# Kernel tuning notes

Hardware: AMD Instinct MI355X
Metric: run time of the kernel (lower is better)

Reference implementation:

```python
import jax, jax.numpy as jnp
import numpy as np
from jax import lax

IN_CH, OUT_CH, K, STYLE_DIM = 512, 512, 3, 512
B, H, W = 16, 64, 64
SCALE = 1.0 / np.sqrt(IN_CH * K * K).astype(np.float32)
EPS = 1e-8


def setup_inputs() -> dict:
    key = jax.random.key(0)
    k1, k2, k3, k4 = jax.random.split(key, 4)
    return {
        "x": jax.random.normal(k1, (B, IN_CH, H, W), dtype=jnp.float32),
        "style": jax.random.normal(k2, (B, STYLE_DIM), dtype=jnp.float32),
        "weight": jax.random.normal(k3, (1, OUT_CH, IN_CH, K, K), dtype=jnp.float32),
        "mod_w": jax.random.normal(k4, (IN_CH, STYLE_DIM), dtype=jnp.float32) / np.sqrt(STYLE_DIM),
        "mod_b": jnp.ones((IN_CH,), dtype=jnp.float32),
    }


def reference(x, style, weight, mod_w, mod_b):
    b, cin, h, w = x.shape
    out_ch = weight.shape[1]
    k = weight.shape[-1]
    pad = k // 2
    # style projection: (B, in_channel)
    s = style @ mod_w.T + mod_b
    # modulated weight: (B, out, in, k, k)
    wmod = SCALE * weight * s[:, None, :, None, None]
    # demodulation: rsqrt of sum of squares over (in, kh, kw)
    demod = lax.rsqrt(jnp.sum(wmod * wmod, axis=(2, 3, 4)) + EPS)
    wmod = wmod * demod[:, :, None, None, None]
    # grouped conv with groups = batch
    wflat = wmod.reshape(b * out_ch, cin, k, k)
    xin = x.reshape(1, b * cin, h, w)
    out = lax.conv_general_dilated(
        xin, wflat,
        window_strides=(1, 1),
        padding=[(pad, pad), (pad, pad)],
        dimension_numbers=("NCHW", "OIHW", "NCHW"),
        feature_group_count=b,
    )
    return out.reshape(b, out_ch, h, w)
```

## Files before the change

kernel.cpp:

```cpp
#include <hip/hip_runtime.h>
#include <hip/hip_bf16.h>
#include <cstdint>
#include <cstddef>

typedef __bf16 bf16x8 __attribute__((ext_vector_type(8)));
typedef float f32x4 __attribute__((ext_vector_type(4)));
typedef float f32x16 __attribute__((ext_vector_type(16)));

#define MOD_SCALE 1.4731391e-02f
#define EPSF 1e-8f

__global__ __launch_bounds__(64) void k_style(
    const float* __restrict__ style, const float* __restrict__ mod_w,
    const float* __restrict__ mod_b, float* __restrict__ s)
{
  __shared__ float st[512];
  const int b = blockIdx.x >> 3, ig = blockIdx.x & 7;
  const int t = threadIdx.x;
  for (int k = t; k < 512; k += 64) st[k] = style[b*512 + k];
  __syncthreads();
  const int i = ig*64 + t;
  const float4* mw = (const float4*)(mod_w + (size_t)i*512);
  float acc = 0.f;
  #pragma unroll 8
  for (int j = 0; j < 128; ++j) {
    float4 v = mw[j];
    acc += v.x*st[4*j] + v.y*st[4*j+1] + v.z*st[4*j+2] + v.w*st[4*j+3];
  }
  s[b*512 + i] = acc + mod_b[i];
}

__global__ __launch_bounds__(256) void k_weight(
    const float* __restrict__ weight, float* __restrict__ w2,
    __hip_bfloat16* __restrict__ Wb)
{
  const int o = blockIdx.x, t = threadIdx.x;
  #pragma unroll
  for (int h = 0; h < 2; ++h) {
    const int i = t + h*256;
    const float* wp = weight + ((size_t)o*512 + i)*9;
    float sq = 0.f;
    #pragma unroll
    for (int kk = 0; kk < 9; ++kk) {
      float v = wp[kk];
      sq += v*v;
      Wb[((size_t)kk*512 + o)*512 + i] = __float2bfloat16(v * MOD_SCALE);
    }
    w2[(size_t)o*512 + i] = sq;
  }
}

__global__ __launch_bounds__(64) void k_demod(
    const float* __restrict__ s, const float* __restrict__ w2,
    float* __restrict__ demod)
{
  __shared__ float s2[512];
  const int b = blockIdx.x >> 3, og = blockIdx.x & 7;
  const int t = threadIdx.x;
  for (int k = t; k < 512; k += 64) { float a = s[b*512 + k]; s2[k] = a*a; }
  __syncthreads();
  const int o = og*64 + t;
  const float4* wp = (const float4*)(w2 + (size_t)o*512);
  float acc = 0.f;
  #pragma unroll 8
  for (int j = 0; j < 128; ++j) {
    float4 v = wp[j];
    acc += v.x*s2[4*j] + v.y*s2[4*j+1] + v.z*s2[4*j+2] + v.w*s2[4*j+3];
  }
  demod[b*512 + o] = rsqrtf(MOD_SCALE*MOD_SCALE*acc + EPSF);
}

__global__ __launch_bounds__(256) void k_xm(
    const float* __restrict__ x, const float* __restrict__ s,
    __hip_bfloat16* __restrict__ Xm)
{
  __shared__ __hip_bfloat16 T[64][72];
  const int bid = blockIdx.x;
  const int cb = bid & 7, y = (bid >> 3) & 63, b = bid >> 9;
  const int ic0 = cb*64;
  const int t = threadIdx.x;
  const int i = t >> 2;
  const int q = t & 3;
  const int x0 = q*16;
  const float sv = s[b*512 + ic0 + i];
  const float4* xp = (const float4*)(x + (size_t)(b*512 + ic0 + i)*4096 + y*64 + x0);
  float4 v[4] = {xp[0], xp[1], xp[2], xp[3]};
  __hip_bfloat16 tmp[16];
  #pragma unroll
  for (int j = 0; j < 4; ++j) {
    tmp[4*j+0] = __float2bfloat16(((const float*)&v[j])[0]*sv);
    tmp[4*j+1] = __float2bfloat16(((const float*)&v[j])[1]*sv);
    tmp[4*j+2] = __float2bfloat16(((const float*)&v[j])[2]*sv);
    tmp[4*j+3] = __float2bfloat16(((const float*)&v[j])[3]*sv);
  }
  *(float4*)&T[i][x0]     = *(const float4*)&tmp[0];
  *(float4*)&T[i][x0 + 8] = *(const float4*)&tmp[8];

  const float4 z4 = make_float4(0.f, 0.f, 0.f, 0.f);
  if (t < 16) {
    const int side = t >> 3, j = t & 7;
    float4* hz = (float4*)(Xm + (((size_t)(b*66 + (y+1))*66 + side*65)*512 + ic0 + j*8));
    *hz = z4;
  }
  if (y == 0) {
    for (int idx = t; idx < 528; idx += 256) {
      const int px = idx >> 3, j = idx & 7;
      float4* hz = (float4*)(Xm + (((size_t)(b*66 + 0)*66 + px)*512 + ic0 + j*8));
      *hz = z4;
    }
  }
  if (y == 63) {
    for (int idx = t; idx < 528; idx += 256) {
      const int px = idx >> 3, j = idx & 7;
      float4* hz = (float4*)(Xm + (((size_t)(b*66 + 65)*66 + px)*512 + ic0 + j*8));
      *hz = z4;
    }
  }

  __syncthreads();
  const int p = t >> 2;
  __hip_bfloat16 o16[16];
  #pragma unroll
  for (int cc = 0; cc < 16; ++cc) o16[cc] = T[q*16 + cc][p];
  __hip_bfloat16* dst = Xm + (((size_t)(b*66 + (y+1))*66 + (p+1))*512 + ic0 + q*16);
  *(float4*)dst       = *(const float4*)&o16[0];
  *(float4*)(dst + 8) = *(const float4*)&o16[8];
}

#define VMC(n) asm volatile("s_waitcnt vmcnt(" #n ")" ::: "memory")

__global__ __launch_bounds__(512, 2) void k_conv(
    const __hip_bfloat16* __restrict__ Wb,
    const __hip_bfloat16* __restrict__ Xm,
    const float* __restrict__ demod,
    float* __restrict__ out)
{
  __shared__ __hip_bfloat16 lds[2][2][16384];

  const int orig = blockIdx.x;
  const int swz = (orig & 7)*64 + (orig >> 3);
  const int b  = swz >> 5;
  const int nt = (swz & 31) >> 1;
  const int mt = swz & 1;
  const int o0 = mt*256, y0 = nt*4;

  const int tid = threadIdx.x;
  const int l = tid & 63;
  const int w = tid >> 6;
  const int wm = w >> 2;
  const int wn = w & 3;

  const int srow = tid >> 3;
  const int tq   = (tid & 7) ^ (srow & 7);
  const char* WbC = (const char*)Wb;
  const char* XmC = (const char*)Xm;

  int aoff[2], boff[2], ldst[2];
  #pragma unroll
  for (int it = 0; it < 2; ++it) {
    const int R  = it*64 + srow;
    const int gr = (R & 0x6F) | ((tq & 1) << 4);
    const int gc = ((tq & 6) | ((R >> 4) & 1)) << 4;
    aoff[it] = (o0 + gr)*1024 + gc;
    boff[it] = (((b*66 + y0 + 1 + (gr >> 6))*66) + (gr & 63) + 1)*1024 + gc;
    ldst[it] = it*8192 + w*1024;
  }

  const int rowb = ((l >> 5) << 4) | (l & 15);
  const int lb4  = (l >> 4) & 1;
  const int sB   = (l & 7) << 4;

  #define STAGE_A(tau, h, bfi) do { \
    const int u_ = ((tau) >> 3)*524288 + (h)*131072 + (((tau) & 7) << 7); \
    _Pragma("unroll") \
    for (int it_ = 0; it_ < 2; ++it_) \
      __builtin_amdgcn_global_load_lds( \
        (__attribute__((address_space(1))) void*)(WbC + u_ + aoff[it_]), \
        (__attribute__((address_space(3))) void*)((char*)&lds[bfi][0][0] + (h)*16384 + ldst[it_]), \
        16, 0, 0); \
  } while(0)

  #define STAGE_B(tau, h, bfi) do { \
    const int kk_ = (tau) >> 3; \
    const int dy_ = kk_/3 - 1, dx_ = kk_ - (kk_/3)*3 - 1; \
    const int u_ = (((h)*2 + dy_)*66 + dx_)*1024 + (((tau) & 7) << 7); \
    _Pragma("unroll") \
    for (int it_ = 0; it_ < 2; ++it_) \
      __builtin_amdgcn_global_load_lds( \
        (__attribute__((address_space(1))) void*)(XmC + u_ + boff[it_]), \
        (__attribute__((address_space(3))) void*)((char*)&lds[bfi][1][0] + (h)*16384 + ldst[it_]), \
        16, 0, 0); \
  } while(0)

  #define RD_A(Ab, MH, dst) do { \
    _Pragma("unroll") \
    for (int mi_ = 0; mi_ < 2; ++mi_) \
      _Pragma("unroll") \
      for (int ks_ = 0; ks_ < 4; ++ks_) \
        dst[mi_][ks_] = *(const bf16x8*)((Ab) + (MH)*16384 + wm*8192 + mi_*4096 \
            + rowb*128 + (((((ks_<<1)|lb4)) << 4) ^ sB)); \
  } while(0)

  #define RD_B(Bb, NH, dst) do { \
    _Pragma("unroll") \
    for (int ks_ = 0; ks_ < 4; ++ks_) \
      dst[ks_] = *(const bf16x8*)((Bb) + (NH)*16384 + wn*4096 \
          + rowb*128 + (((((ks_<<1)|lb4)) << 4) ^ sB)); \
  } while(0)

  #define MFMAQ(AM0, dstA, NH, dstB) do { \
    _Pragma("unroll") \
    for (int ks_ = 0; ks_ < 4; ++ks_) \
      _Pragma("unroll") \
      for (int mi_ = 0; mi_ < 2; ++mi_) \
        acc[(AM0)+mi_][NH] = __builtin_amdgcn_mfma_f32_32x32x16_bf16( \
            dstA[mi_][ks_], dstB[ks_], acc[(AM0)+mi_][NH], 0, 0, 0); \
  } while(0)

  #define TILE(BFI, S1, S2, S3, S4, VM1, VM4) do { \
    const char* Ab_ = (const char*)&lds[BFI][0][0]; \
    const char* Bb_ = (const char*)&lds[BFI][1][0]; \
    bf16x8 a0_[2][4], a1_[2][4], b0_[4], b1_[4]; \
     \
    RD_A(Ab_, 0, a0_); RD_B(Bb_, 0, b0_); \
    S1; \
    __builtin_amdgcn_s_barrier(); \
    __builtin_amdgcn_s_setprio(1); MFMAQ(0, a0_, 0, b0_); __builtin_amdgcn_s_setprio(0); \
    VM1; \
    __builtin_amdgcn_s_barrier(); \
     \
    RD_B(Bb_, 1, b1_); \
    S2; \
    __builtin_amdgcn_s_barrier(); \
    __builtin_amdgcn_s_setprio(1); MFMAQ(0, a0_, 1, b1_); __builtin_amdgcn_s_setprio(0); \
    __builtin_amdgcn_s_barrier(); \
     \
    RD_A(Ab_, 1, a1_); \
    S3; \
    __builtin_amdgcn_s_barrier(); \
    __builtin_amdgcn_s_setprio(1); MFMAQ(2, a1_, 1, b1_); __builtin_amdgcn_s_setprio(0); \
    __builtin_amdgcn_s_barrier(); \
     \
    S4; \
    __builtin_amdgcn_s_barrier(); \
    __builtin_amdgcn_s_setprio(1); MFMAQ(2, a1_, 0, b0_); __builtin_amdgcn_s_setprio(0); \
    VM4; \
    __builtin_amdgcn_s_barrier(); \
  } while(0)

  f32x16 acc[4][2] = {};

  STAGE_A(0, 0, 0); STAGE_A(0, 1, 0); STAGE_B(0, 0, 0); STAGE_B(0, 1, 0);
  STAGE_B(1, 0, 1); STAGE_A(1, 1, 1);
  VMC(4);
  __builtin_amdgcn_s_barrier();

  #pragma unroll 1
  for (int tt = 0; tt < 35; ++tt) {
    const int t = tt*2;
    TILE(0, STAGE_A(t+1,0,1), STAGE_B(t+1,1,1), STAGE_B(t+2,0,0), STAGE_A(t+2,1,0),
            VMC(6), VMC(6));
    TILE(1, STAGE_A(t+2,0,0), STAGE_B(t+2,1,0), STAGE_B(t+3,0,1), STAGE_A(t+3,1,1),
            VMC(6), VMC(6));
  }
  TILE(0, STAGE_A(71,0,1), STAGE_B(71,1,1), (void)0, (void)0, VMC(6), VMC(2));
  TILE(1, (void)0, (void)0, (void)0, (void)0, VMC(0), (void)0);

  const int lr = l & 31;
  #pragma unroll
  for (int am = 0; am < 4; ++am) {
    const int om = o0 + (am >> 1)*128 + wm*64 + (am & 1)*32 + ((l >> 5) << 2);
    #pragma unroll
    for (int NH = 0; NH < 2; ++NH) {
      const int nc = NH*128 + wn*32 + lr;
      const int y = y0 + (nc >> 6), xx = nc & 63;
      #pragma unroll
      for (int g = 0; g < 4; ++g) {
        const f32x4 dm = *(const f32x4*)(demod + b*512 + om + 8*g);
        float* op = out + (size_t)(b*512 + om + 8*g)*4096 + y*64 + xx;
        #pragma unroll
        for (int j = 0; j < 4; ++j)
          op[(size_t)j*4096] = acc[am][NH][g*4 + j] * dm[j];
      }
    }
  }
  #undef TILE
  #undef MFMAQ
  #undef RD_A
  #undef RD_B
  #undef STAGE_A
  #undef STAGE_B
}

extern "C" void kernel_launch(void* const* d_in, const int* in_sizes, int n_in,
                              void* d_out, int out_size, void* d_ws, size_t ws_size,
                              hipStream_t stream)
{
  const float* x      = (const float*)d_in[0];
  const float* style  = (const float*)d_in[1];
  const float* weight = (const float*)d_in[2];
  const float* mod_w  = (const float*)d_in[3];
  const float* mod_b  = (const float*)d_in[4];
  float* out = (float*)d_out;

  char* ws = (char*)d_ws;
  float* s            = (float*)(ws);
  float* demod        = (float*)(ws + 32768);
  float* w2           = (float*)(ws + 65536);
  __hip_bfloat16* Wb  = (__hip_bfloat16*)(ws + 1114112);
  __hip_bfloat16* Xm  = (__hip_bfloat16*)(ws + 5832704);

  k_style <<<128,  64, 0, stream>>>(style, mod_w, mod_b, s);
  k_weight<<<512, 256, 0, stream>>>(weight, w2, Wb);
  k_demod <<<128,  64, 0, stream>>>(s, w2, demod);
  k_xm    <<<8192, 256, 0, stream>>>(x, s, Xm);
  k_conv  <<<512,  512, 0, stream>>>(Wb, Xm, demod, out);
}
```

Before: 352.6 us.

## Replace 256x256 conv GEMM tile with simpler 128x256 tile using 16x16 MFMA

Rewrites the main conv kernel to use 256-thread blocks computing 128 output channels by 256 pixels, with 16x16x32 MFMAs, a K-step of 32, and a simple double-buffered loop that waits for all loads and barriers every step. The grid is doubled to 1024 blocks. The old 512-thread, 256x256 tile with swizzled LDS, interleaved partial stages and priority hints is removed. This reduces register pressure and code complexity, but it also loses data reuse per block, adds bank conflicts from the unswizzled LDS layout, and puts a full vmcnt(0) wait plus a barrier in every one of the 144 iterations, so load latency is less hidden.

Result: slower. 369.8 us (+4.9%).

```diff
diff --git a/kernel.cpp b/kernel.cpp
--- a/kernel.cpp
+++ b/kernel.cpp
@@ -5,7 +5,6 @@
 
 typedef __bf16 bf16x8 __attribute__((ext_vector_type(8)));
 typedef float f32x4 __attribute__((ext_vector_type(4)));
-typedef float f32x16 __attribute__((ext_vector_type(16)));
 
 #define MOD_SCALE 1.4731391e-02f
 #define EPSF 1e-8f
@@ -129,167 +128,108 @@
 
 #define VMC(n) asm volatile("s_waitcnt vmcnt(" #n ")" ::: "memory")
 
-__global__ __launch_bounds__(512, 2) void k_conv(
+__global__ __launch_bounds__(256, 2) void k_conv(
     const __hip_bfloat16* __restrict__ Wb,
     const __hip_bfloat16* __restrict__ Xm,
     const float* __restrict__ demod,
     float* __restrict__ out)
 {
-  __shared__ __hip_bfloat16 lds[2][2][16384];
+  __shared__ __hip_bfloat16 lds[2][12288];
 
   const int orig = blockIdx.x;
-  const int swz = (orig & 7)*64 + (orig >> 3);
-  const int b  = swz >> 5;
-  const int nt = (swz & 31) >> 1;
-  const int mt = swz & 1;
-  const int o0 = mt*256, y0 = nt*4;
-
-  const int tid = threadIdx.x;
-  const int l = tid & 63;
-  const int w = tid >> 6;
-  const int wm = w >> 2;
-  const int wn = w & 3;
-
-  const int srow = tid >> 3;
-  const int tq   = (tid & 7) ^ (srow & 7);
+  const int swz = (orig & 7)*128 + (orig >> 3);
+  const int b  = swz >> 6;
+  const int mt = (swz >> 4) & 3;
+  const int nt = swz & 15;
+  const int o0 = mt*128, y0 = nt*4;
+
+  const int t = threadIdx.x;
+  const int l = t & 63;
+  const int w = t >> 6;
+
   const char* WbC = (const char*)Wb;
   const char* XmC = (const char*)Xm;
 
-  int aoff[2], boff[2], ldst[2];
-  #pragma unroll
-  for (int it = 0; it < 2; ++it) {
-    const int R  = it*64 + srow;
-    const int gr = (R & 0x6F) | ((tq & 1) << 4);
-    const int gc = ((tq & 6) | ((R >> 4) & 1)) << 4;
-    aoff[it] = (o0 + gr)*1024 + gc;
-    boff[it] = (((b*66 + y0 + 1 + (gr >> 6))*66) + (gr & 63) + 1)*1024 + gc;
-    ldst[it] = it*8192 + w*1024;
-  }
-
-  const int rowb = ((l >> 5) << 4) | (l & 15);
-  const int lb4  = (l >> 4) & 1;
-  const int sB   = (l & 7) << 4;
-
-  #define STAGE_A(tau, h, bfi) do { \
-    const int u_ = ((tau) >> 3)*524288 + (h)*131072 + (((tau) & 7) << 7); \
+  int aoff[2], boff[4];
+  #pragma unroll
+  for (int it = 0; it < 2; ++it)
+    aoff[it] = (o0 + it*64 + (t >> 2))*1024 + (t & 3)*16;
+  #pragma unroll
+  for (int it = 0; it < 4; ++it)
+    boff[it] = ((b*66 + y0 + 1 + it)*66 + (t >> 2) + 1)*1024 + (t & 3)*16;
+
+  const int fr  = l & 15;
+  const int kq  = (l >> 4) << 4;
+
+  #define STAGE(tau, bfi) do { \
+    const int ua_ = ((tau) >> 4)*524288 + (((tau) & 15) << 6); \
+    const int kk_ = (tau) >> 4; \
+    const int dy_ = kk_/3 - 1, dx_ = kk_ - (kk_/3)*3 - 1; \
+    const int ub_ = (dy_*66 + dx_)*1024 + (((tau) & 15) << 6); \
     _Pragma("unroll") \
     for (int it_ = 0; it_ < 2; ++it_) \
       __builtin_amdgcn_global_load_lds( \
-        (__attribute__((address_space(1))) void*)(WbC + u_ + aoff[it_]), \
-        (__attribute__((address_space(3))) void*)((char*)&lds[bfi][0][0] + (h)*16384 + ldst[it_]), \
+        (__attribute__((address_space(1))) void*)(WbC + ua_ + aoff[it_]), \
+        (__attribute__((address_space(3))) void*)((char*)&lds[bfi][0] + it_*4096 + w*1024), \
+        16, 0, 0); \
+    _Pragma("unroll") \
+    for (int it_ = 0; it_ < 4; ++it_) \
+      __builtin_amdgcn_global_load_lds( \
+        (__attribute__((address_space(1))) void*)(XmC + ub_ + boff[it_]), \
+        (__attribute__((address_space(3))) void*)((char*)&lds[bfi][0] + 8192 + it_*4096 + w*1024), \
         16, 0, 0); \
   } while(0)
 
-  #define STAGE_B(tau, h, bfi) do { \
-    const int kk_ = (tau) >> 3; \
-    const int dy_ = kk_/3 - 1, dx_ = kk_ - (kk_/3)*3 - 1; \
-    const int u_ = (((h)*2 + dy_)*66 + dx_)*1024 + (((tau) & 7) << 7); \
-    _Pragma("unroll") \
-    for (int it_ = 0; it_ < 2; ++it_) \
-      __builtin_amdgcn_global_load_lds( \
-        (__attribute__((address_space(1))) void*)(XmC + u_ + boff[it_]), \
-        (__attribute__((address_space(3))) void*)((char*)&lds[bfi][1][0] + (h)*16384 + ldst[it_]), \
-        16, 0, 0); \
+  #define COMPUTE(bfi) do { \
+    const char* Ab_ = (const char*)&lds[bfi][0]; \
+    const char* Bb_ = Ab_ + 8192; \
+    bf16x8 a_[8], b_[4]; \
+    _Pragma("unroll") \
+    for (int mi_ = 0; mi_ < 8; ++mi_) \
+      a_[mi_] = *(const bf16x8*)(Ab_ + (mi_*16 + fr)*64 + kq); \
+    _Pragma("unroll") \
+    for (int ni_ = 0; ni_ < 4; ++ni_) \
+      b_[ni_] = *(const bf16x8*)(Bb_ + (w*64 + ni_*16 + fr)*64 + kq); \
+    _Pragma("unroll") \
+    for (int mi_ = 0; mi_ < 8; ++mi_) \
+      _Pragma("unroll") \
+      for (int ni_ = 0; ni_ < 4; ++ni_) \
+        acc[mi_][ni_] = __builtin_amdgcn_mfma_f32_16x16x32_bf16( \
+            a_[mi_], b_[ni_], acc[mi_][ni_], 0, 0, 0); \
   } while(0)
 
-  #define RD_A(Ab, MH, dst) do { \
-    _Pragma("unroll") \
-    for (int mi_ = 0; mi_ < 2; ++mi_) \
-      _Pragma("unroll") \
-      for (int ks_ = 0; ks_ < 4; ++ks_) \
-        dst[mi_][ks_] = *(const bf16x8*)((Ab) + (MH)*16384 + wm*8192 + mi_*4096 \
-            + rowb*128 + (((((ks_<<1)|lb4)) << 4) ^ sB)); \
-  } while(0)
-
-  #define RD_B(Bb, NH, dst) do { \
-    _Pragma("unroll") \
-    for (int ks_ = 0; ks_ < 4; ++ks_) \
-      dst[ks_] = *(const bf16x8*)((Bb) + (NH)*16384 + wn*4096 \
-          + rowb*128 + (((((ks_<<1)|lb4)) << 4) ^ sB)); \
-  } while(0)
-
-  #define MFMAQ(AM0, dstA, NH, dstB) do { \
-    _Pragma("unroll") \
-    for (int ks_ = 0; ks_ < 4; ++ks_) \
-      _Pragma("unroll") \
-      for (int mi_ = 0; mi_ < 2; ++mi_) \
-        acc[(AM0)+mi_][NH] = __builtin_amdgcn_mfma_f32_32x32x16_bf16( \
-            dstA[mi_][ks_], dstB[ks_], acc[(AM0)+mi_][NH], 0, 0, 0); \
-  } while(0)
-
-  #define TILE(BFI, S1, S2, S3, S4, VM1, VM4) do { \
-    const char* Ab_ = (const char*)&lds[BFI][0][0]; \
-    const char* Bb_ = (const char*)&lds[BFI][1][0]; \
-    bf16x8 a0_[2][4], a1_[2][4], b0_[4], b1_[4]; \
-     \
-    RD_A(Ab_, 0, a0_); RD_B(Bb_, 0, b0_); \
-    S1; \
-    __builtin_amdgcn_s_barrier(); \
-    __builtin_amdgcn_s_setprio(1); MFMAQ(0, a0_, 0, b0_); __builtin_amdgcn_s_setprio(0); \
-    VM1; \
-    __builtin_amdgcn_s_barrier(); \
-     \
-    RD_B(Bb_, 1, b1_); \
-    S2; \
-    __builtin_amdgcn_s_barrier(); \
-    __builtin_amdgcn_s_setprio(1); MFMAQ(0, a0_, 1, b1_); __builtin_amdgcn_s_setprio(0); \
-    __builtin_amdgcn_s_barrier(); \
-     \
-    RD_A(Ab_, 1, a1_); \
-    S3; \
-    __builtin_amdgcn_s_barrier(); \
-    __builtin_amdgcn_s_setprio(1); MFMAQ(2, a1_, 1, b1_); __builtin_amdgcn_s_setprio(0); \
-    __builtin_amdgcn_s_barrier(); \
-     \
-    S4; \
-    __builtin_amdgcn_s_barrier(); \
-    __builtin_amdgcn_s_setprio(1); MFMAQ(2, a1_, 0, b0_); __builtin_amdgcn_s_setprio(0); \
-    VM4; \
-    __builtin_amdgcn_s_barrier(); \
-  } while(0)
-
-  f32x16 acc[4][2] = {};
-
-  STAGE_A(0, 0, 0); STAGE_A(0, 1, 0); STAGE_B(0, 0, 0); STAGE_B(0, 1, 0);
-  STAGE_B(1, 0, 1); STAGE_A(1, 1, 1);
-  VMC(4);
+  f32x4 acc[8][4] = {};
+
+  STAGE(0, 0);
+  VMC(0);
   __builtin_amdgcn_s_barrier();
 
-  #pragma unroll 1
-  for (int tt = 0; tt < 35; ++tt) {
-    const int t = tt*2;
-    TILE(0, STAGE_A(t+1,0,1), STAGE_B(t+1,1,1), STAGE_B(t+2,0,0), STAGE_A(t+2,1,0),
-            VMC(6), VMC(6));
-    TILE(1, STAGE_A(t+2,0,0), STAGE_B(t+2,1,0), STAGE_B(t+3,0,1), STAGE_A(t+3,1,1),
-            VMC(6), VMC(6));
-  }
-  TILE(0, STAGE_A(71,0,1), STAGE_B(71,1,1), (void)0, (void)0, VMC(6), VMC(2));
-  TILE(1, (void)0, (void)0, (void)0, (void)0, VMC(0), (void)0);
-
-  const int lr = l & 31;
-  #pragma unroll
-  for (int am = 0; am < 4; ++am) {
-    const int om = o0 + (am >> 1)*128 + wm*64 + (am & 1)*32 + ((l >> 5) << 2);
+  #pragma unroll 2
+  for (int tau = 0; tau < 143; ++tau) {
+    const int p = tau & 1;
+    STAGE(tau + 1, p ^ 1);
+    COMPUTE(p);
+    VMC(0);
+    __builtin_amdgcn_s_barrier();
+  }
+  COMPUTE(1);
+
+  #pragma unroll
+  for (int mi = 0; mi < 8; ++mi) {
+    const int om = o0 + mi*16 + ((l >> 4) << 2);
+    const f32x4 dm = *(const f32x4*)(demod + b*512 + om);
     #pragma unroll
-    for (int NH = 0; NH < 2; ++NH) {
-      const int nc = NH*128 + wn*32 + lr;
+    for (int ni = 0; ni < 4; ++ni) {
+      const int nc = w*64 + ni*16 + (l & 15);
       const int y = y0 + (nc >> 6), xx = nc & 63;
+      float* op = out + (size_t)(b*512 + om)*4096 + y*64 + xx;
       #pragma unroll
-      for (int g = 0; g < 4; ++g) {
-        const f32x4 dm = *(const f32x4*)(demod + b*512 + om + 8*g);
-        float* op = out + (size_t)(b*512 + om + 8*g)*4096 + y*64 + xx;
-        #pragma unroll
-        for (int j = 0; j < 4; ++j)
-          op[(size_t)j*4096] = acc[am][NH][g*4 + j] * dm[j];
-      }
-    }
-  }
-  #undef TILE
-  #undef MFMAQ
-  #undef RD_A
-  #undef RD_B
-  #undef STAGE_A
-  #undef STAGE_B
+      for (int j = 0; j < 4; ++j)
+        op[(size_t)j*4096] = acc[mi][ni][j] * dm[j];
+    }
+  }
+  #undef COMPUTE
+  #undef STAGE
 }
 
 extern "C" void kernel_launch(void* const* d_in, const int* in_sizes, int n_in,
@@ -314,5 +254,5 @@
   k_weight<<<512, 256, 0, stream>>>(weight, w2, Wb);
   k_demod <<<128,  64, 0, stream>>>(s, w2, demod);
   k_xm    <<<8192, 256, 0, stream>>>(x, s, Xm);
-  k_conv  <<<512,  512, 0, stream>>>(Wb, Xm, demod, out);
-}
+  k_conv  <<<1024, 256, 0, stream>>>(Wb, Xm, demod, out);
+}
```
